# Kernel optimization log

Hardware: AMD Instinct MI355X
Metric: run time of the kernel (lower is better)

Reference implementation:

```python
import jax, jax.numpy as jnp
import numpy as np
from jax import lax

WIN = 9
PAD = WIN // 2

def _box_avg(x):
    s = lax.reduce_window(
        x, 0.0, lax.add,
        window_dimensions=(1, 1, WIN, WIN),
        window_strides=(1, 1, 1, 1),
        padding=[(0, 0), (0, 0), (PAD, PAD), (PAD, PAD)],
    )
    return s / float(WIN * WIN)


def setup_inputs() -> dict:
    key = jax.random.key(0)
    k1, k2 = jax.random.split(key)
    I = jax.random.normal(k1, (32, 1, 512, 512), dtype=jnp.float32)
    J = jax.random.normal(k2, (32, 1, 512, 512), dtype=jnp.float32)
    return {"I": I, "J": J}


def reference(I, J):
    I_mean = _box_avg(I)
    J_mean = _box_avg(J)
    dI = I - I_mean
    dJ = J - J_mean
    I_var = _box_avg(dI * dI)
    J_var = _box_avg(dJ * dJ)
    IJ_cov = _box_avg(dI * dJ)
    ncc = (IJ_cov * IJ_cov) / (I_var * J_var + 1e-5)
    return -jnp.mean(ncc)
```

## Files before the change

kernel.cpp:

```cpp
#include <hip/hip_runtime.h>


constexpr int BATCH = 32;
constexpr int H = 512, W = 512;
constexpr int YB = 16;
constexpr int NBAND = H / YB;
constexpr float EPS81 = 81.0f * 81.0f * 1e-5f;

using h2 = __attribute__((ext_vector_type(2))) _Float16;

__global__ void zero_accum(float* ws) { ws[0] = 0.0f; }

__device__ __forceinline__ h2 up1(h2 x) {
  return __builtin_bit_cast(
      h2, __builtin_amdgcn_update_dpp(0, __builtin_bit_cast(int, x), 0x138, 0xF,
                                      0xF, true));
}
__device__ __forceinline__ h2 dn1(h2 x) {
  return __builtin_bit_cast(
      h2, __builtin_amdgcn_update_dpp(0, __builtin_bit_cast(int, x), 0x130, 0xF,
                                      0xF, true));
}
__device__ __forceinline__ h2 pkm(float lo, float hi, unsigned m) {
  const unsigned u =
      __builtin_bit_cast(unsigned, __builtin_amdgcn_cvt_pkrtz(lo, hi)) & m;
  return __builtin_bit_cast(h2, u);
}
__device__ __forceinline__ h2 swp(h2 x) {
  return __builtin_shufflevector(x, x, 1, 0);
}

__device__ __forceinline__ void tap8(const h2 u[8], h2 O[8]) {
  const h2 P0 = u[0], P1 = P0 + u[1], P2 = P1 + u[2], P3 = P2 + u[3],
           P4 = P3 + u[4], P5 = P4 + u[5], P6 = P5 + u[6], T = P6 + u[7];
  const h2 UP3 = up1(P3), UP4 = up1(P4), UP5 = up1(P5), UP6 = up1(P6), UT = up1(T);
  const h2 DP0 = dn1(P0), DP1 = dn1(P1), DP2 = dn1(P2), DP3 = dn1(P3);
  O[0] = (UT - UP3) + P4;
  O[1] = (UT - UP4) + P5;
  O[2] = (UT - UP5) + P6;
  O[3] = (UT - UP6) + T;
  O[4] = T + DP0;
  O[5] = (T - P0) + DP1;
  O[6] = (T - P1) + DP2;
  O[7] = (T - P2) + DP3;
}

__global__ __launch_bounds__(64, 1) void ncc_stream(const float* __restrict__ I,
                                                    const float* __restrict__ J,
                                                    float* __restrict__ accum) {
  const int lane = threadIdx.x;
  const int blk = blockIdx.x;
  const int band = blk & (NBAND - 1);
  const int b = blk >> 5;
  const int yb = band * YB;
  const int x0 = 8 * lane;
  const h2 zero2 = {_Float16(0.0f), _Float16(0.0f)};
  const h2 ninv81 = {_Float16(-1.0f / 81.0f), _Float16(-1.0f / 81.0f)};

  const float* __restrict__ Ib = I + (size_t)b * (H * W);
  const float* __restrict__ Jb = J + (size_t)b * (H * W);

  h2 rg[9][8];
  h2 d9[9][8];
  h2 V[8];
  h2 vpq[8];
  h2 vr[8];
#pragma unroll
  for (int s = 0; s < 9; ++s)
#pragma unroll
    for (int c = 0; c < 8; ++c) { rg[s][c] = zero2; d9[s][c] = zero2; }
#pragma unroll
  for (int c = 0; c < 8; ++c) { V[c] = zero2; vpq[c] = zero2; vr[c] = zero2; }
  float acc = 0.f;

  float4 bI0[6], bI1[6], bJ0[6], bJ1[6];
#pragma unroll
  for (int j = 0; j < 6; ++j) {
    const int y0 = yb - 8 + j;
    const int yc0 = y0 < 0 ? 0 : (y0 > H - 1 ? H - 1 : y0);
    const int off0 = yc0 * W + x0;
    bI0[j] = *reinterpret_cast<const float4*>(Ib + off0);
    bI1[j] = *reinterpret_cast<const float4*>(Ib + off0 + 4);
    bJ0[j] = *reinterpret_cast<const float4*>(Jb + off0);
    bJ1[j] = *reinterpret_cast<const float4*>(Jb + off0 + 4);
  }

#pragma unroll 1
  for (int ch = 0; ch < 2; ++ch) {
#pragma unroll
    for (int si2 = 0; si2 < 18; ++si2) {
      const int k = ch * 18 + si2;
      if (k < 32) {
        const int si = si2 % 9;
        const int t = (si + 5) % 9;
        const int sl = si2 % 6;
        const int y = yb - 8 + k;
        const unsigned msk = ((y >= 0) & (y < H)) ? 0xFFFFFFFFu : 0u;

        h2 na[8];
        na[0] = pkm(bI0[sl].x, bJ0[sl].x, msk);
        na[1] = pkm(bI0[sl].y, bJ0[sl].y, msk);
        na[2] = pkm(bI0[sl].z, bJ0[sl].z, msk);
        na[3] = pkm(bI0[sl].w, bJ0[sl].w, msk);
        na[4] = pkm(bI1[sl].x, bJ1[sl].x, msk);
        na[5] = pkm(bI1[sl].y, bJ1[sl].y, msk);
        na[6] = pkm(bI1[sl].z, bJ1[sl].z, msk);
        na[7] = pkm(bI1[sl].w, bJ1[sl].w, msk);

        {
          const int yn = y + 6;
          const int ycn = yn < 0 ? 0 : (yn > H - 1 ? H - 1 : yn);
          const int offn = ycn * W + x0;
          bI0[sl] = *reinterpret_cast<const float4*>(Ib + offn);
          bI1[sl] = *reinterpret_cast<const float4*>(Ib + offn + 4);
          bJ0[sl] = *reinterpret_cast<const float4*>(Jb + offn);
          bJ1[sl] = *reinterpret_cast<const float4*>(Jb + offn + 4);
        }

#pragma unroll
        for (int c = 0; c < 8; ++c) {
          V[c] += na[c] - rg[si][c];
          rg[si][c] = na[c];
        }

        if (k >= 8) {
          const int m = y - 4;
          if ((m >= 0) & (m < H)) {
            h2 M[8];
            tap8(V, M);
#pragma unroll
            for (int c = 0; c < 8; ++c) {
              const h2 d = M[c] * ninv81 + rg[t][c];
              const h2 o = d9[t][c];
              vpq[c] += d * d - o * o;
              vr[c] += d * swp(d) - o * swp(o);
              d9[t][c] = d;
            }
          } else {
#pragma unroll
            for (int c = 0; c < 8; ++c) {
              const h2 o = d9[t][c];
              vpq[c] -= o * o;
              vr[c] -= o * swp(o);
              d9[t][c] = zero2;
            }
          }

          if (k >= 16) {
            h2 P[8], R[8];
            tap8(vpq, P);
            tap8(vr, R);
#pragma unroll
            for (int c = 0; c < 8; ++c) {
              const float Pl = (float)P[c][0], Qh = (float)P[c][1];
              const float Rl = (float)R[c][0];
              acc += (Rl * Rl) * __builtin_amdgcn_rcpf(fmaf(Pl, Qh, EPS81));
            }
          }
        }
      }
    }
  }

#pragma unroll
  for (int off = 32; off > 0; off >>= 1) acc += __shfl_down(acc, off, 64);
  if (lane == 0) atomicAdd(accum, acc);
}

__global__ void finalize(const float* __restrict__ ws, float* __restrict__ out) {
  out[0] = -ws[0] * (1.0f / (float)((size_t)BATCH * H * W));
}

extern "C" void kernel_launch(void* const* d_in, const int* in_sizes, int n_in,
                              void* d_out, int out_size, void* d_ws, size_t ws_size,
                              hipStream_t stream) {
  const float* I = (const float*)d_in[0];
  const float* J = (const float*)d_in[1];
  float* out = (float*)d_out;
  float* acc = (float*)d_ws;

  zero_accum<<<1, 1, 0, stream>>>(acc);
  ncc_stream<<<BATCH * NBAND, 64, 0, stream>>>(I, J, acc);
  finalize<<<1, 1, 0, stream>>>(acc, out);
}
```

Measured before the change: 43.76 us.

## Fully unroll row stream, use explicit vmcnt prefetch pipeline and LDS history ring

Replaces the two-chunk loop with a compile-time fully unrolled sequence of 32 steps. Global loads are now issued through inline asm with explicit s_waitcnt vmcnt thresholds, and the prefetch depth drops from 6 rows to 4. The 9-row history of centered values moves from registers into LDS, indexed per lane. The aim is lower VGPR pressure and more precise overlap of memory with compute. The cost is LDS traffic on every step, a shallower prefetch window, and sched barriers that constrain the compiler's scheduling.

```diff
diff --git a/kernel.cpp b/kernel.cpp
--- a/kernel.cpp
+++ b/kernel.cpp
@@ -1,13 +1,18 @@
 #include <hip/hip_runtime.h>
+#include <utility>
 
 
 constexpr int BATCH = 32;
 constexpr int H = 512, W = 512;
 constexpr int YB = 16;
 constexpr int NBAND = H / YB;
+constexpr int NSTEP = YB + 16;
+constexpr int PFD = 4;
 constexpr float EPS81 = 81.0f * 81.0f * 1e-5f;
 
 using h2 = __attribute__((ext_vector_type(2))) _Float16;
+using f4 = __attribute__((ext_vector_type(4))) float;
+using u4 = __attribute__((ext_vector_type(4))) unsigned int;
 
 __global__ void zero_accum(float* ws) { ws[0] = 0.0f; }
 
@@ -28,6 +33,26 @@
 }
 __device__ __forceinline__ h2 swp(h2 x) {
   return __builtin_shufflevector(x, x, 1, 0);
+}
+
+__device__ __forceinline__ void gload2(const float* p, f4& a, f4& b) {
+  asm volatile(
+      "global_load_dwordx4 %0, %2, off\n\t"
+      "global_load_dwordx4 %1, %2, off offset:16"
+      : "=&v"(a), "=&v"(b)
+      : "v"(p));
+}
+
+template <int N>
+__device__ __forceinline__ void waitcnt_vm() {
+  asm volatile("s_waitcnt vmcnt(%0)" ::"i"(N) : "memory");
+  __builtin_amdgcn_sched_barrier(0);
+}
+
+template <class F, int... Ks>
+__device__ __forceinline__ void unroll_steps(F&& f,
+                                             std::integer_sequence<int, Ks...>) {
+  (f(std::integral_constant<int, Ks>{}), ...);
 }
 
 __device__ __forceinline__ void tap8(const h2 u[8], h2 O[8]) {
@@ -60,42 +85,49 @@
   const float* __restrict__ Ib = I + (size_t)b * (H * W);
   const float* __restrict__ Jb = J + (size_t)b * (H * W);
 
+  __shared__ u4 d9s[9][2][64];
+
   h2 rg[9][8];
-  h2 d9[9][8];
   h2 V[8];
   h2 vpq[8];
   h2 vr[8];
 #pragma unroll
   for (int s = 0; s < 9; ++s)
 #pragma unroll
-    for (int c = 0; c < 8; ++c) { rg[s][c] = zero2; d9[s][c] = zero2; }
+    for (int c = 0; c < 8; ++c) rg[s][c] = zero2;
 #pragma unroll
   for (int c = 0; c < 8; ++c) { V[c] = zero2; vpq[c] = zero2; vr[c] = zero2; }
+  const u4 zero4 = {0u, 0u, 0u, 0u};
+#pragma unroll
+  for (int s = 0; s < 9; ++s) {
+    d9s[s][0][lane] = zero4;
+    d9s[s][1][lane] = zero4;
+  }
   float acc = 0.f;
 
-  float4 bI0[6], bI1[6], bJ0[6], bJ1[6];
-#pragma unroll
-  for (int j = 0; j < 6; ++j) {
+  f4 bI0[PFD], bI1[PFD], bJ0[PFD], bJ1[PFD];
+
+#pragma unroll
+  for (int j = 0; j < PFD; ++j) {
     const int y0 = yb - 8 + j;
-    const int yc0 = y0 < 0 ? 0 : (y0 > H - 1 ? H - 1 : y0);
+    const int yc0 = y0 < 0 ? 0 : y0;
     const int off0 = yc0 * W + x0;
-    bI0[j] = *reinterpret_cast<const float4*>(Ib + off0);
-    bI1[j] = *reinterpret_cast<const float4*>(Ib + off0 + 4);
-    bJ0[j] = *reinterpret_cast<const float4*>(Jb + off0);
-    bJ1[j] = *reinterpret_cast<const float4*>(Jb + off0 + 4);
+    gload2(Ib + off0, bI0[j], bI1[j]);
+    gload2(Jb + off0, bJ0[j], bJ1[j]);
   }
 
-#pragma unroll 1
-  for (int ch = 0; ch < 2; ++ch) {
-#pragma unroll
-    for (int si2 = 0; si2 < 18; ++si2) {
-      const int k = ch * 18 + si2;
-      if (k < 32) {
-        const int si = si2 % 9;
-        const int t = (si + 5) % 9;
-        const int sl = si2 % 6;
-        const int y = yb - 8 + k;
+  unroll_steps(
+      [&](auto kc) {
+        constexpr int K = decltype(kc)::value;
+        constexpr int si = K % 9;
+        constexpr int t = (si + 5) % 9;
+        constexpr int sl = K % PFD;
+        constexpr int REM = NSTEP - 1 - K;
+        constexpr int ALW = (REM < PFD - 1 ? REM : PFD - 1) * 4;
+        const int y = yb - 8 + K;
         const unsigned msk = ((y >= 0) & (y < H)) ? 0xFFFFFFFFu : 0u;
+
+        waitcnt_vm<ALW>();
 
         h2 na[8];
         na[0] = pkm(bI0[sl].x, bJ0[sl].x, msk);
@@ -107,14 +139,12 @@
         na[6] = pkm(bI1[sl].z, bJ1[sl].z, msk);
         na[7] = pkm(bI1[sl].w, bJ1[sl].w, msk);
 
-        {
-          const int yn = y + 6;
+        if constexpr (K + PFD < NSTEP) {
+          const int yn = y + PFD;
           const int ycn = yn < 0 ? 0 : (yn > H - 1 ? H - 1 : yn);
           const int offn = ycn * W + x0;
-          bI0[sl] = *reinterpret_cast<const float4*>(Ib + offn);
-          bI1[sl] = *reinterpret_cast<const float4*>(Ib + offn + 4);
-          bJ0[sl] = *reinterpret_cast<const float4*>(Jb + offn);
-          bJ1[sl] = *reinterpret_cast<const float4*>(Jb + offn + 4);
+          gload2(Ib + offn, bI0[sl], bI1[sl]);
+          gload2(Jb + offn, bJ0[sl], bJ1[sl]);
         }
 
 #pragma unroll
@@ -123,30 +153,39 @@
           rg[si][c] = na[c];
         }
 
-        if (k >= 8) {
+        if constexpr (K >= 8) {
           const int m = y - 4;
+          const u4 ov0 = d9s[t][0][lane];
+          const u4 ov1 = d9s[t][1][lane];
           if ((m >= 0) & (m < H)) {
             h2 M[8];
             tap8(V, M);
+            u4 nv0, nv1;
 #pragma unroll
             for (int c = 0; c < 8; ++c) {
               const h2 d = M[c] * ninv81 + rg[t][c];
-              const h2 o = d9[t][c];
+              const h2 o =
+                  __builtin_bit_cast(h2, c < 4 ? ov0[c] : ov1[c - 4]);
               vpq[c] += d * d - o * o;
               vr[c] += d * swp(d) - o * swp(o);
-              d9[t][c] = d;
+              const unsigned du = __builtin_bit_cast(unsigned, d);
+              if (c < 4) nv0[c] = du; else nv1[c - 4] = du;
             }
+            d9s[t][0][lane] = nv0;
+            d9s[t][1][lane] = nv1;
           } else {
 #pragma unroll
             for (int c = 0; c < 8; ++c) {
-              const h2 o = d9[t][c];
+              const h2 o =
+                  __builtin_bit_cast(h2, c < 4 ? ov0[c] : ov1[c - 4]);
               vpq[c] -= o * o;
               vr[c] -= o * swp(o);
-              d9[t][c] = zero2;
             }
+            d9s[t][0][lane] = zero4;
+            d9s[t][1][lane] = zero4;
           }
 
-          if (k >= 16) {
+          if constexpr (K >= 16) {
             h2 P[8], R[8];
             tap8(vpq, P);
             tap8(vr, R);
@@ -158,9 +197,8 @@
             }
           }
         }
-      }
-    }
-  }
+      },
+      std::make_integer_sequence<int, NSTEP>{});
 
 #pragma unroll
   for (int off = 32; off > 0; off >>= 1) acc += __shfl_down(acc, off, 64);
```

Result: slower. 53.66 us (+22.6%).
